# Kernel tuning notes

Measured on AMD Instinct MI355X. Metric: run time of the kernel, lower is better.

Reference implementation:

```python
import jax, jax.numpy as jnp
import numpy as np

ALPHA = 0.2  # LeakyReLU negative slope


def setup_inputs() -> dict:
    key = jax.random.key(0)
    k1, k2, k3 = jax.random.split(key, 3)
    B, N, F_in, F_out = 8, 2048, 256, 256
    h = jax.random.normal(k1, (B, N, F_in), dtype=jnp.float32)
    adj = jax.random.randint(k2, (B, N, N), 0, 2, dtype=jnp.int32)
    # xavier_uniform for W [F_in, F_out]
    limit = float(np.sqrt(6.0 / (F_in + F_out)))
    W = jax.random.uniform(k3, (F_in, F_out), dtype=jnp.float32, minval=-limit, maxval=limit)
    return {"h": h, "adj": adj, "W": W}


def reference(h, adj, W):
    # h: [B,N,F_in], W: [F_in,F_out] -> Wh: [B,N,F_out]
    Wh = jnp.einsum('bnf,fo->bno', h, W)
    # (Wh_i + Wh_j).sum(-1) == s[p] + s[q] with s = Wh.sum(-1); avoids [B,N,N,F] tensor
    s = Wh.sum(axis=-1)  # [B,N]
    e = jax.nn.leaky_relu(s[:, :, None] + s[:, None, :], negative_slope=ALPHA)  # [B,N,N]
    e = jnp.where(adj == 0, -jnp.inf, e)
    alpha = jax.nn.softmax(e, axis=-1)  # masked softmax over neighbors
    # dropout is identity in eval mode
    h_prime = jnp.einsum('bpq,bqo->bpo', alpha, Wh)  # [B,N,F_out]
    return h_prime
```

## Files before the change

kernel.cpp:

```cpp
#include <hip/hip_runtime.h>
#include <hip/hip_bf16.h>
#include <stdint.h>

#define LEAKY_ALPHA 0.2f

using f32x4 = __attribute__((ext_vector_type(4))) float;
using u32x2 = __attribute__((ext_vector_type(2))) unsigned int;
using u32x4 = __attribute__((ext_vector_type(4))) unsigned int;
using i32x4 = __attribute__((ext_vector_type(4))) int;
using s16x8 = __attribute__((ext_vector_type(8))) short;

static __device__ __forceinline__ unsigned short f2bf(float x) {
  __hip_bfloat16 b = __float2bfloat16(x);
  return __builtin_bit_cast(unsigned short, b);
}

__global__ __launch_bounds__(256) void gat_prep(
    const float* __restrict__ W, __hip_bfloat16* __restrict__ WT,
    float* __restrict__ wsum)
{
  const int o = blockIdx.x;
  const int t = threadIdx.x;
  WT[o * 256 + t] = __float2bfloat16(W[t * 256 + o]);
  float u = W[o * 256 + t];
#pragma unroll
  for (int off = 1; off < 64; off <<= 1) u += __shfl_xor(u, off, 64);
  __shared__ float red[4];
  if ((t & 63) == 0) red[t >> 6] = u;
  __syncthreads();
  if (t == 0) wsum[o] = red[0] + red[1] + red[2] + red[3];
}

__global__ __launch_bounds__(256) void gat_wh2(
    const float* __restrict__ h, const __hip_bfloat16* __restrict__ WT,
    const float* __restrict__ wsum, __hip_bfloat16* __restrict__ WhT,
    float* __restrict__ s)
{
  const int b = blockIdx.x >> 5;
  const int q0 = (blockIdx.x & 31) * 64;
  const int t = threadIdx.x;
  const int wid = t >> 6, lane = t & 63;

  __shared__ __align__(16) unsigned char Bh[64 * 512];
  __shared__ __align__(16) unsigned char Aw[256 * 128];
  __shared__ __align__(16) float wsl[256];

  wsl[t] = wsum[t];
  __syncthreads();

  {
    const int q = t >> 2;
    const int fs = (t & 3) * 64;
    const float* hrow = h + ((size_t)(b * 2048 + q0 + q)) * 256 + fs;
    float sp = 0.f;
#pragma unroll
    for (int c = 0; c < 8; ++c) {
      const f32x4 a  = *(const f32x4*)&hrow[c * 8];
      const f32x4 bq = *(const f32x4*)&hrow[c * 8 + 4];
      const f32x4 wa = *(const f32x4*)&wsl[fs + c * 8];
      const f32x4 wb = *(const f32x4*)&wsl[fs + c * 8 + 4];
      sp += a[0]*wa[0] + a[1]*wa[1] + a[2]*wa[2] + a[3]*wa[3]
          + bq[0]*wb[0] + bq[1]*wb[1] + bq[2]*wb[2] + bq[3]*wb[3];
      u32x4 pk;
      pk[0] = (unsigned)f2bf(a[0])  | ((unsigned)f2bf(a[1])  << 16);
      pk[1] = (unsigned)f2bf(a[2])  | ((unsigned)f2bf(a[3])  << 16);
      pk[2] = (unsigned)f2bf(bq[0]) | ((unsigned)f2bf(bq[1]) << 16);
      pk[3] = (unsigned)f2bf(bq[2]) | ((unsigned)f2bf(bq[3]) << 16);
      const int boff = q * 512 + ((fs * 2 + c * 16) ^ ((q & 7) << 4));
      *(u32x4*)&Bh[boff] = pk;
    }
    sp += __shfl_xor(sp, 1, 64);
    sp += __shfl_xor(sp, 2, 64);
    if ((t & 3) == 0) s[b * 2048 + q0 + q] = sp;
  }

  f32x4 acc[4][4];
#pragma unroll
  for (int i = 0; i < 4; ++i)
#pragma unroll
    for (int j = 0; j < 4; ++j) acc[i][j] = (f32x4)(0.f);

  for (int it = 0; it < 4; ++it) {
    const int f0 = it * 64;
    __syncthreads();
#pragma unroll
    for (int j = 0; j < 8; ++j) {
      const int o = (t >> 3) + 32 * j;
      const int c = t & 7;
      const u32x4 v = *(const u32x4*)&WT[o * 256 + f0 + c * 8];
      *(u32x4*)&Aw[o * 128 + ((c * 16) ^ ((o & 7) << 4))] = v;
    }
    __syncthreads();
#pragma unroll
    for (int kt = 0; kt < 2; ++kt) {
      const int kb = kt * 64 + ((lane >> 4) << 4);
      s16x8 af[4], bf[4];
#pragma unroll
      for (int qt = 0; qt < 4; ++qt) {
        const int qr = qt * 16 + (lane & 15);
        af[qt] = *(const s16x8*)&Bh[qr * 512 + ((f0 * 2 + kb) ^ ((qr & 7) << 4))];
      }
#pragma unroll
      for (int ot = 0; ot < 4; ++ot) {
        const int orow = wid * 64 + ot * 16 + (lane & 15);
        bf[ot] = *(const s16x8*)&Aw[orow * 128 + (kb ^ ((orow & 7) << 4))];
      }
#pragma unroll
      for (int qt = 0; qt < 4; ++qt)
#pragma unroll
        for (int ot = 0; ot < 4; ++ot)
          acc[qt][ot] = __builtin_amdgcn_mfma_f32_16x16x32_bf16(
              af[qt], bf[ot], acc[qt][ot], 0, 0, 0);
    }
  }

  __hip_bfloat16* __restrict__ WhTb = WhT + (size_t)b * 256 * 2048;
#pragma unroll
  for (int qt = 0; qt < 4; ++qt)
#pragma unroll
    for (int ot = 0; ot < 4; ++ot) {
      const int o = wid * 64 + ot * 16 + (lane & 15);
      const int ql = q0 + qt * 16 + ((lane >> 4) << 2);
      u32x2 pk;
      pk[0] = (unsigned)f2bf(acc[qt][ot][0]) | ((unsigned)f2bf(acc[qt][ot][1]) << 16);
      pk[1] = (unsigned)f2bf(acc[qt][ot][2]) | ((unsigned)f2bf(acc[qt][ot][3]) << 16);
      *(u32x2*)&WhTb[(size_t)o * 2048 + ql] = pk;
    }
}

__global__ __launch_bounds__(512, 4) void gat_attn(
    const int* __restrict__ adj, const float* __restrict__ s,
    const __hip_bfloat16* __restrict__ WhT, float* __restrict__ out)
{
  const int N = 2048;
  const int bid = blockIdx.x;
  const int swz = (bid & 7) * 64 + (bid >> 3);
  const int b = swz >> 6;
  const int p0 = (swz & 63) * 32;
  const int t = threadIdx.x;
  const int wid = t >> 6, lane = t & 63;

  __shared__ __align__(16) unsigned char Bs[2][256 * 128];
  __shared__ __align__(16) unsigned char Wt[2][32 * 128];
  __shared__ __align__(16) float red_sh[8];
  __shared__ __align__(16) float l_sh[32];

  const int ep = t >> 4;
  const int eq4 = (t & 15) * 4;
  const int* __restrict__ adjrow = adj + ((size_t)(b * N + p0 + ep)) * N;
  const float* __restrict__ sB = s + b * N;
  const __hip_bfloat16* __restrict__ WhTb = WhT + (size_t)b * 256 * 2048;

  const int so = t >> 3;
  const int q16 = t & 7;

  const f32x4 s4 = *(const f32x4*)&sB[t * 4];
  float bm = fmaxf(fmaxf(s4[0], s4[1]), fmaxf(s4[2], s4[3]));
#pragma unroll
  for (int off = 1; off < 64; off <<= 1) bm = fmaxf(bm, __shfl_xor(bm, off, 64));
  if (lane == 0) red_sh[wid] = bm;
  const float s_p = sB[p0 + ep];
  __syncthreads();
  float smax = red_sh[0];
#pragma unroll
  for (int k = 1; k < 8; ++k) smax = fmaxf(smax, red_sh[k]);
  const float xm = s_p + smax;
  const float m_p = (xm > 0.f) ? xm : (LEAKY_ALPHA * xm);

  f32x4 acc[2][2];
#pragma unroll
  for (int pt = 0; pt < 2; ++pt)
#pragma unroll
    for (int ot = 0; ot < 2; ++ot) acc[pt][ot] = (f32x4)(0.f);
  float lacc = 0.f;

  u32x4 breg[4];
#pragma unroll
  for (int j = 0; j < 4; ++j)
    breg[j] = *(const u32x4*)&WhTb[(size_t)(so + 64 * j) * 2048 + q16 * 8];

  i32x4 aE = *(const i32x4*)&adjrow[eq4];
  f32x4 sE = *(const f32x4*)&sB[eq4];
  i32x4 aO = *(const i32x4*)&adjrow[64 + eq4];
  f32x4 sO = *(const f32x4*)&sB[64 + eq4];

  const int wtoff = ep * 128 + ((eq4 * 2) ^ ((ep & 7) << 4));

  auto tile = [&](int BI, int QQ, i32x4& AV, f32x4& SV) __attribute__((always_inline)) {
    float wv[4];
#pragma unroll
    for (int i = 0; i < 4; ++i) {
      const float x = s_p + SV[i];
      const float le = (x > 0.f) ? x : (LEAKY_ALPHA * x);
      const float w = __expf(le - m_p);
      wv[i] = (AV[i] != 0) ? w : 0.f;
      lacc += wv[i];
    }
    {
      u32x2 pw;
      pw[0] = (unsigned)f2bf(wv[0]) | ((unsigned)f2bf(wv[1]) << 16);
      pw[1] = (unsigned)f2bf(wv[2]) | ((unsigned)f2bf(wv[3]) << 16);
      *(u32x2*)&Wt[BI][wtoff] = pw;
    }
#pragma unroll
    for (int j = 0; j < 4; ++j) {
      const int o = so + 64 * j;
      *(u32x4*)&Bs[BI][o * 128 + ((q16 * 16) ^ ((o & 7) << 4))] = breg[j];
    }
    if (QQ + 64 < N) {
#pragma unroll
      for (int j = 0; j < 4; ++j)
        breg[j] = *(const u32x4*)&WhTb[(size_t)(so + 64 * j) * 2048 +
                                       QQ + 64 + q16 * 8];
    }
    if (QQ + 128 < N) {
      AV = *(const i32x4*)&adjrow[QQ + 128 + eq4];
      SV = *(const f32x4*)&sB[QQ + 128 + eq4];
    }
    asm volatile("s_waitcnt lgkmcnt(0)" ::: "memory");
    __builtin_amdgcn_s_barrier();
    asm volatile("" ::: "memory");
    {
      s16x8 afr[2][2], bfr[2][2];
#pragma unroll
      for (int pt = 0; pt < 2; ++pt)
#pragma unroll
        for (int kt = 0; kt < 2; ++kt) {
          const int pa = pt * 16 + (lane & 15);
          const int kb = kt * 64 + ((lane >> 4) << 4);
          afr[pt][kt] = *(const s16x8*)&Wt[BI][pa * 128 + (kb ^ ((pa & 7) << 4))];
        }
#pragma unroll
      for (int ot = 0; ot < 2; ++ot)
#pragma unroll
        for (int kt = 0; kt < 2; ++kt) {
          const int ob = wid * 32 + ot * 16 + (lane & 15);
          const int kb = kt * 64 + ((lane >> 4) << 4);
          bfr[ot][kt] = *(const s16x8*)&Bs[BI][ob * 128 + (kb ^ ((ob & 7) << 4))];
        }
      __builtin_amdgcn_s_setprio(1);
#pragma unroll
      for (int pt = 0; pt < 2; ++pt)
#pragma unroll
        for (int ot = 0; ot < 2; ++ot)
#pragma unroll
          for (int kt = 0; kt < 2; ++kt)
            acc[pt][ot] = __builtin_amdgcn_mfma_f32_16x16x32_bf16(
                afr[pt][kt], bfr[ot][kt], acc[pt][ot], 0, 0, 0);
      __builtin_amdgcn_s_setprio(0);
    }
  };

  for (int q0 = 0; q0 < N; q0 += 128) {
    tile(0, q0, aE, sE);
    tile(1, q0 + 64, aO, sO);
  }

  lacc += __shfl_xor(lacc, 1, 64);
  lacc += __shfl_xor(lacc, 2, 64);
  lacc += __shfl_xor(lacc, 4, 64);
  lacc += __shfl_xor(lacc, 8, 64);
  if ((t & 15) == 0) l_sh[ep] = lacc;
  __syncthreads();

#pragma unroll
  for (int pt = 0; pt < 2; ++pt) {
    const f32x4 lv = *(const f32x4*)&l_sh[pt * 16 + ((lane >> 4) << 2)];
    f32x4 inv;
#pragma unroll
    for (int r = 0; r < 4; ++r) inv[r] = 1.f / lv[r];
#pragma unroll
    for (int ot = 0; ot < 2; ++ot) {
      const int o = wid * 32 + ot * 16 + (lane & 15);
#pragma unroll
      for (int r = 0; r < 4; ++r) {
        const int row = p0 + pt * 16 + ((lane >> 4) << 2) + r;
        out[((size_t)(b * N + row)) * 256 + o] = acc[pt][ot][r] * inv[r];
      }
    }
  }
}

extern "C" void kernel_launch(void* const* d_in, const int* in_sizes, int n_in,
                              void* d_out, int out_size, void* d_ws, size_t ws_size,
                              hipStream_t stream) {
  const float* h = (const float*)d_in[0];
  const int* adj = (const int*)d_in[1];
  const float* W = (const float*)d_in[2];
  float* out = (float*)d_out;

  char* ws = (char*)d_ws;
  __hip_bfloat16* WhT = (__hip_bfloat16*)ws;
  float* s = (float*)(ws + (size_t)8 * 1024 * 1024);
  __hip_bfloat16* WT = (__hip_bfloat16*)(ws + (size_t)8 * 1024 * 1024 + 65536);
  float* wsum = (float*)(ws + (size_t)8 * 1024 * 1024 + 65536 + 131072);

  gat_prep<<<256, 256, 0, stream>>>(W, WT, wsum);
  gat_wh2<<<256, 256, 0, stream>>>(h, WT, wsum, WhT, s);
  gat_attn<<<512, 512, 0, stream>>>(adj, s, WhT, out);
}
```

Baseline: 57.84 us.

## Stream WhT tiles directly into LDS via global_load_lds double buffering

Replaces the register-staged copy of WhT tiles (global load into VGPRs, then ds_write into swizzled LDS) with direct global-to-LDS loads, with the XOR swizzle applied on the global source address instead. The next tile is prefetched into the other LDS buffer right after the barrier, and vmcnt waiting keeps the adjacency and s loads overlapped. The aim is to cut VGPR pressure and ds_write traffic. In exchange it relies on a precise vmcnt count and issues redundant clamped loads on the final iterations.

```diff
diff --git a/kernel.cpp b/kernel.cpp
--- a/kernel.cpp
+++ b/kernel.cpp
@@ -151,8 +151,23 @@
   const float* __restrict__ sB = s + b * N;
   const __hip_bfloat16* __restrict__ WhTb = WhT + (size_t)b * 256 * 2048;
 
-  const int so = t >> 3;
-  const int q16 = t & 7;
+  const int grow = t >> 3;
+  const int gchunk = t & 7;
+  const size_t gsrc_off = (size_t)grow * 2048 + (size_t)((gchunk ^ (grow & 7)) << 3);
+  const int ldst = wid * 1024;
+
+  const int wtoff = ep * 128 + ((eq4 * 2) ^ ((ep & 7) << 4));
+
+#pragma unroll
+  for (int c = 0; c < 4; ++c)
+    __builtin_amdgcn_global_load_lds(
+        (const __attribute__((address_space(1))) unsigned int*)(WhTb + gsrc_off + (size_t)c * 64 * 2048),
+        (__attribute__((address_space(3))) unsigned int*)&Bs[0][c * 8192 + ldst],
+        16, 0, 0);
+  i32x4 aE = *(const i32x4*)&adjrow[eq4];
+  f32x4 sE = *(const f32x4*)&sB[eq4];
+  i32x4 aO = *(const i32x4*)&adjrow[64 + eq4];
+  f32x4 sO = *(const f32x4*)&sB[64 + eq4];
 
   const f32x4 s4 = *(const f32x4*)&sB[t * 4];
   float bm = fmaxf(fmaxf(s4[0], s4[1]), fmaxf(s4[2], s4[3]));
@@ -173,18 +188,6 @@
 #pragma unroll
     for (int ot = 0; ot < 2; ++ot) acc[pt][ot] = (f32x4)(0.f);
   float lacc = 0.f;
-
-  u32x4 breg[4];
-#pragma unroll
-  for (int j = 0; j < 4; ++j)
-    breg[j] = *(const u32x4*)&WhTb[(size_t)(so + 64 * j) * 2048 + q16 * 8];
-
-  i32x4 aE = *(const i32x4*)&adjrow[eq4];
-  f32x4 sE = *(const f32x4*)&sB[eq4];
-  i32x4 aO = *(const i32x4*)&adjrow[64 + eq4];
-  f32x4 sO = *(const f32x4*)&sB[64 + eq4];
-
-  const int wtoff = ep * 128 + ((eq4 * 2) ^ ((ep & 7) << 4));
 
   auto tile = [&](int BI, int QQ, i32x4& AV, f32x4& SV) __attribute__((always_inline)) {
     float wv[4];
@@ -202,24 +205,24 @@
       pw[1] = (unsigned)f2bf(wv[2]) | ((unsigned)f2bf(wv[3]) << 16);
       *(u32x2*)&Wt[BI][wtoff] = pw;
     }
-#pragma unroll
-    for (int j = 0; j < 4; ++j) {
-      const int o = so + 64 * j;
-      *(u32x4*)&Bs[BI][o * 128 + ((q16 * 16) ^ ((o & 7) << 4))] = breg[j];
-    }
-    if (QQ + 64 < N) {
-#pragma unroll
-      for (int j = 0; j < 4; ++j)
-        breg[j] = *(const u32x4*)&WhTb[(size_t)(so + 64 * j) * 2048 +
-                                       QQ + 64 + q16 * 8];
-    }
-    if (QQ + 128 < N) {
-      AV = *(const i32x4*)&adjrow[QQ + 128 + eq4];
-      SV = *(const f32x4*)&sB[QQ + 128 + eq4];
-    }
-    asm volatile("s_waitcnt lgkmcnt(0)" ::: "memory");
+    {
+      const int qr = (QQ + 128 < N) ? (QQ + 128) : (N - 64);
+      AV = *(const i32x4*)&adjrow[qr + eq4];
+      SV = *(const f32x4*)&sB[qr + eq4];
+    }
+    asm volatile("s_waitcnt vmcnt(2) lgkmcnt(0)" ::: "memory");
     __builtin_amdgcn_s_barrier();
-    asm volatile("" ::: "memory");
+    __builtin_amdgcn_sched_barrier(0);
+    {
+      const int qg = (QQ + 64 < N) ? (QQ + 64) : (N - 64);
+      const __hip_bfloat16* gs = WhTb + qg + gsrc_off;
+#pragma unroll
+      for (int c = 0; c < 4; ++c)
+        __builtin_amdgcn_global_load_lds(
+            (const __attribute__((address_space(1))) unsigned int*)(gs + (size_t)c * 64 * 2048),
+            (__attribute__((address_space(3))) unsigned int*)&Bs[BI ^ 1][c * 8192 + ldst],
+            16, 0, 0);
+    }
     {
       s16x8 afr[2][2], bfr[2][2];
 #pragma unroll
```

Result: slower. 61.12 us (+5.7%).
